# Performance work log

Hardware: AMD Instinct MI355X
Metric: run time of the kernel (lower is better)

The kernel has to match this reference:

```python
import jax, jax.numpy as jnp
import numpy as np

K = 8192  # particles
T = 4096  # timesteps
LOG2PI = float(np.log(2.0 * np.pi))


def _normal_logpdf(x, mu):
    # Normal(mu, 1).log_prob(x)
    return -0.5 * (x - mu) ** 2 - 0.5 * LOG2PI


def setup_inputs() -> dict:
    key = jax.random.key(0)
    k1, k2, k3, k4 = jax.random.split(key, 4)
    x = jax.random.normal(k1, (T,), dtype=jnp.float32)          # observations
    w0 = jax.random.normal(k2, (K,), dtype=jnp.float32)          # Pw=N(0,1) samples
    z = jax.random.normal(k3, (K, T), dtype=jnp.float32)         # Qz=N(0,1) samples
    u = jax.random.uniform(k4, (T, K), dtype=jnp.float32)        # resampling uniforms
    return {"x": x, "w0": w0, "z": z, "u": u}


def reference(x, w0, z, u):
    # Precompute terms that the torch code computes once before the loop.
    log_Qz = _normal_logpdf(z, 0.0)                 # [K, T]  q.Qz().log_prob(z)
    log_PxGz = _normal_logpdf(x[None, :], z)        # [K, T]  p.PxGz(z).log_prob(x)
    delta = log_PxGz - log_Qz                       # [K, T]
    logK = jnp.log(jnp.asarray(K, dtype=z.dtype))

    def step(w, inp):
        z_t, d_t, u_t = inp                         # each [K]
        # log_ws = p.PzGw(w).log_prob(z_t) + log_PxGz_t - log_Qz_t
        log_ws = _normal_logpdf(z_t, w) + d_t       # [K]
        lme = jax.nn.logsumexp(log_ws) - logK       # logmeanexp over particles
        # Categorical(logits=log_ws).sample([K]) via inverse-CDF with uniforms
        cdf = jnp.cumsum(jax.nn.softmax(log_ws))    # [K]
        idx = jnp.clip(jnp.searchsorted(cdf, u_t), 0, K - 1)  # [K]
        return w[idx], lme                          # resample: w = w[idx]

    _, res = jax.lax.scan(step, w0, (z.T, delta.T, u))  # scan over T timesteps
    return jnp.sum(res)
```

## Files before the change

### kernel.cpp

```cpp
#include <hip/hip_runtime.h>
#include <math.h>

#define KP 8192
#define TSTEPS 4096
#define BLOCK 1024
#define PT 8
#define NWAVES 16
#define NBUCK 8192
#define NBF 8192.0f
#define MSTEPS 16
#define F_INF __int_as_float(0x7f800000)

template <int CTRL, int RM>
__device__ __forceinline__ float dpp_add_f(float x) {
  int s = __builtin_amdgcn_update_dpp(0, __float_as_int(x), CTRL, RM, 0xF, false);
  return x + __int_as_float(s);
}
template <int CTRL, int RM>
__device__ __forceinline__ int dpp_add_i(int x) {
  int s = __builtin_amdgcn_update_dpp(0, x, CTRL, RM, 0xF, false);
  return x + s;
}
template <int CTRL, int RM>
__device__ __forceinline__ int dpp_max_i(int x) {
  int s = __builtin_amdgcn_update_dpp(0, x, CTRL, RM, 0xF, false);
  return x > s ? x : s;
}
__device__ __forceinline__ float wscan64_add(float x) {
  x = dpp_add_f<0x111, 0xF>(x); x = dpp_add_f<0x112, 0xF>(x);
  x = dpp_add_f<0x114, 0xF>(x); x = dpp_add_f<0x118, 0xF>(x);
  x = dpp_add_f<0x142, 0xA>(x); x = dpp_add_f<0x143, 0xC>(x);
  return x;
}
__device__ __forceinline__ int wscan64_addi(int x) {
  x = dpp_add_i<0x111, 0xF>(x); x = dpp_add_i<0x112, 0xF>(x);
  x = dpp_add_i<0x114, 0xF>(x); x = dpp_add_i<0x118, 0xF>(x);
  x = dpp_add_i<0x142, 0xA>(x); x = dpp_add_i<0x143, 0xC>(x);
  return x;
}
__device__ __forceinline__ int wscan64_max(int x) {
  x = dpp_max_i<0x111, 0xF>(x); x = dpp_max_i<0x112, 0xF>(x);
  x = dpp_max_i<0x114, 0xF>(x); x = dpp_max_i<0x118, 0xF>(x);
  x = dpp_max_i<0x142, 0xA>(x); x = dpp_max_i<0x143, 0xC>(x);
  return x;
}
__device__ __forceinline__ float rscan16_add(float x) {
  x = dpp_add_f<0x111, 0xF>(x); x = dpp_add_f<0x112, 0xF>(x);
  x = dpp_add_f<0x114, 0xF>(x); x = dpp_add_f<0x118, 0xF>(x);
  return x;
}
__device__ __forceinline__ int rscan16_addi(int x) {
  x = dpp_add_i<0x111, 0xF>(x); x = dpp_add_i<0x112, 0xF>(x);
  x = dpp_add_i<0x114, 0xF>(x); x = dpp_add_i<0x118, 0xF>(x);
  return x;
}
__device__ __forceinline__ int rscan16_max(int x) {
  x = dpp_max_i<0x111, 0xF>(x); x = dpp_max_i<0x112, 0xF>(x);
  x = dpp_max_i<0x114, 0xF>(x); x = dpp_max_i<0x118, 0xF>(x);
  return x;
}
__device__ __forceinline__ float readlane_f(float v, int l) {
  return __int_as_float(__builtin_amdgcn_readlane(__float_as_int(v), l));
}

__global__ void transpose_k(const float* __restrict__ in, float* __restrict__ out) {
  __shared__ float tile[32][33];
  const int c0 = blockIdx.x * 32;
  const int r0 = blockIdx.y * 32;
  const int tx = threadIdx.x;
  const int ty = threadIdx.y;
#pragma unroll
  for (int i = 0; i < 32; i += 8)
    tile[ty + i][tx] = in[(size_t)(r0 + ty + i) * TSTEPS + c0 + tx];
  __syncthreads();
#pragma unroll
  for (int i = 0; i < 32; i += 8)
    out[(size_t)(c0 + ty + i) * KP + r0 + tx] = tile[tx][ty + i];
}

__global__ __launch_bounds__(BLOCK) void sortu_k(const float* __restrict__ u,
                                                 float* __restrict__ su,
                                                 unsigned short* __restrict__ rnk) {
  __shared__ int hist[NBUCK];
  __shared__ float sval[KP];
  __shared__ unsigned short sidx[KP];
  __shared__ int redi[NWAVES];
  const int t = blockIdx.x;
  const int tid = threadIdx.x;
  const int lane = tid & 63;
  const int wid = tid >> 6;
  const int kbase = tid * PT;

  float uv[PT];
  {
    float4 a = *(const float4*)(u + (size_t)t * KP + kbase);
    float4 b = *(const float4*)(u + (size_t)t * KP + kbase + 4);
    uv[0] = a.x; uv[1] = a.y; uv[2] = a.z; uv[3] = a.w;
    uv[4] = b.x; uv[5] = b.y; uv[6] = b.z; uv[7] = b.w;
  }
  int bj[PT];
#pragma unroll
  for (int j = 0; j < PT; ++j) {
    int b = (int)(uv[j] * NBF);
    bj[j] = b > NBUCK - 1 ? NBUCK - 1 : b;
  }
  {
    int4 z4; z4.x = z4.y = z4.z = z4.w = 0;
    *(int4*)(hist + kbase) = z4;
    *(int4*)(hist + kbase + 4) = z4;
  }
  __syncthreads();
#pragma unroll
  for (int j = 0; j < PT; ++j) atomicAdd(&hist[bj[j]], 1);
  __syncthreads();

  int4 ha = *(const int4*)(hist + kbase);
  int4 hb = *(const int4*)(hist + kbase + 4);
  int c0 = ha.x, c1 = c0 + ha.y, c2 = c1 + ha.z, c3 = c2 + ha.w;
  int c4 = c3 + hb.x, c5 = c4 + hb.y, c6 = c5 + hb.z, c7 = c6 + hb.w;
  int wincl = wscan64_addi(c7);
  int wexcl = wincl - c7;
  if (lane == 63) redi[wid] = wincl;
  __syncthreads();
  int v16 = rscan16_addi(redi[lane & 15]);
  int cp = wid ? __builtin_amdgcn_readlane(v16, wid - 1) : 0;
  int base = cp + wexcl;
  {
    int4 pa; pa.x = base; pa.y = base + c0; pa.z = base + c1; pa.w = base + c2;
    int4 pb; pb.x = base + c3; pb.y = base + c4; pb.z = base + c5; pb.w = base + c6;
    *(int4*)(hist + kbase) = pa;
    *(int4*)(hist + kbase + 4) = pb;
  }
  __syncthreads();
#pragma unroll
  for (int j = 0; j < PT; ++j) {
    int pos = atomicAdd(&hist[bj[j]], 1);
    sval[pos] = uv[j];
    sidx[pos] = (unsigned short)(kbase + j);
  }
  __syncthreads();
  for (int bb = tid; bb < NBUCK; bb += BLOCK) {
    int s0 = bb ? hist[bb - 1] : 0;
    int e0 = hist[bb];
    for (int m = s0 + 1; m < e0; ++m) {
      float v = sval[m];
      unsigned short ix = sidx[m];
      int p = m - 1;
      while (p >= s0 && sval[p] > v) {
        sval[p + 1] = sval[p];
        sidx[p + 1] = sidx[p];
        --p;
      }
      sval[p + 1] = v;
      sidx[p + 1] = ix;
    }
  }
  __syncthreads();
  {
    float4 a, b;
    a.x = sval[kbase + 0]; a.y = sval[kbase + 1]; a.z = sval[kbase + 2]; a.w = sval[kbase + 3];
    b.x = sval[kbase + 4]; b.y = sval[kbase + 5]; b.z = sval[kbase + 6]; b.w = sval[kbase + 7];
    *(float4*)(su + (size_t)t * KP + kbase) = a;
    *(float4*)(su + (size_t)t * KP + kbase + 4) = b;
  }
#pragma unroll
  for (int j = 0; j < PT; ++j)
    rnk[(size_t)t * KP + sidx[kbase + j]] = (unsigned short)(kbase + j);
}

__global__ __launch_bounds__(BLOCK) void smc_scan3(const float* __restrict__ x,
                                                   const float* __restrict__ w0,
                                                   const float* __restrict__ zsrc,
                                                   const float* __restrict__ su_g,
                                                   const unsigned short* __restrict__ rk_g,
                                                   float* __restrict__ out) {
  extern __shared__ float sm[];
  float* w_s   = sm;
  float* cdf_s = sm + KP;
  float* su_s  = cdf_s + KP + 8;
  float* P_s   = su_s + KP + 8;
  float* redF  = P_s + KP;

  const int tid = threadIdx.x;
  const int lane = tid & 63;
  const int wid = tid >> 6;
  const int kbase = tid * PT;

  if (tid == 0) { cdf_s[KP] = F_INF; su_s[KP] = F_INF; }

  float wv[PT];
  {
    float4 a = *(const float4*)(w0 + kbase);
    float4 b = *(const float4*)(w0 + kbase + 4);
    wv[0] = a.x; wv[1] = a.y; wv[2] = a.z; wv[3] = a.w;
    wv[4] = b.x; wv[5] = b.y; wv[6] = b.z; wv[7] = b.w;
    *(float4*)(w_s + kbase) = a;
    *(float4*)(w_s + kbase + 4) = b;
  }

  float4 zna, znb, sna, snb;
  int4 rkn;
  float xt_next = x[0];
  zna = *(const float4*)(zsrc + kbase);
  znb = *(const float4*)(zsrc + kbase + 4);
  sna = *(const float4*)(su_g + kbase);
  snb = *(const float4*)(su_g + kbase + 4);
  rkn = *(const int4*)(rk_g + kbase);

  float acc = 0.f;

  for (int t = 0; t < TSTEPS; ++t) {
    *(float4*)(su_s + kbase) = sna;
    *(float4*)(su_s + kbase + 4) = snb;
    float zv[PT];
    zv[0] = zna.x; zv[1] = zna.y; zv[2] = zna.z; zv[3] = zna.w;
    zv[4] = znb.x; zv[5] = znb.y; zv[6] = znb.z; zv[7] = znb.w;
    const int4 rkc = rkn;
    const float xt = xt_next;

    if (t + 1 < TSTEPS) {
      xt_next = x[t + 1];
      const size_t ro = (size_t)(t + 1) * KP + kbase;
      zna = *(const float4*)(zsrc + ro);
      znb = *(const float4*)(zsrc + ro + 4);
      sna = *(const float4*)(su_g + ro);
      snb = *(const float4*)(su_g + ro + 4);
      rkn = *(const int4*)(rk_g + ro);
    }

    float s[PT];
    float run = 0.f;
#pragma unroll
    for (int j = 0; j < PT; ++j) {
      float d = zv[j] - wv[j];
      float lw = fmaf(xt, zv[j], -0.5f * d * d);
      run += __expf(lw);
      s[j] = run;
    }
    const float wincl = wscan64_add(run);
    const float wexcl = wincl - run;
    if (lane == 63) redF[wid] = wincl;
    __syncthreads();

    float v16 = rscan16_add(redF[lane & 15]);
    const float total = readlane_f(v16, 15);
    const float wpre = wid ? readlane_f(v16, wid - 1) : 0.f;
    const float base = wpre + wexcl;
    const float invT = 1.0f / total;
    if (tid == 0)
      acc += __logf(total) - 9.0109133472792886f
             - 0.5f * (1.8378770664093453f + xt * xt);
    {
      float4 a, b;
      a.x = (base + s[0]) * invT; a.y = (base + s[1]) * invT;
      a.z = (base + s[2]) * invT; a.w = (base + s[3]) * invT;
      b.x = (base + s[4]) * invT; b.y = (base + s[5]) * invT;
      b.z = (base + s[6]) * invT; b.w = (base + s[7]) * invT;
      *(float4*)(cdf_s + kbase) = a;
      *(float4*)(cdf_s + kbase + 4) = b;
    }
    __syncthreads();

    {
      const int d = tid * MSTEPS;
      int lo = d > KP ? d - KP : 0;
      int hi = d < KP ? d : KP;
      while (lo < hi) {
        const int m = (lo + hi) >> 1;
        const float a = cdf_s[m];
        const float b = su_s[d - 1 - m];
        if (a >= b) hi = m; else lo = m + 1;
      }
      int i = lo;
      int j = d - lo;
      float av = cdf_s[i];
      float bv = su_s[j];
#pragma unroll 1
      for (int sme = 0; sme < MSTEPS; ++sme) {
        const bool cons = (av < bv);
        if (!cons) P_s[j] = w_s[i < KP ? i : KP - 1];
        i += cons ? 1 : 0;
        j += cons ? 0 : 1;
        const float nv = cons ? cdf_s[i] : su_s[j];
        av = cons ? nv : av;
        bv = cons ? bv : nv;
      }
    }
    __syncthreads();

    {
      int r[PT];
      r[0] = rkc.x & 0xffff; r[1] = (rkc.x >> 16) & 0xffff;
      r[2] = rkc.y & 0xffff; r[3] = (rkc.y >> 16) & 0xffff;
      r[4] = rkc.z & 0xffff; r[5] = (rkc.z >> 16) & 0xffff;
      r[6] = rkc.w & 0xffff; r[7] = (rkc.w >> 16) & 0xffff;
#pragma unroll
      for (int j = 0; j < PT; ++j) wv[j] = P_s[r[j]];
      float4 a, b;
      a.x = wv[0]; a.y = wv[1]; a.z = wv[2]; a.w = wv[3];
      b.x = wv[4]; b.y = wv[5]; b.z = wv[6]; b.w = wv[7];
      *(float4*)(w_s + kbase) = a;
      *(float4*)(w_s + kbase + 4) = b;
    }
  }

  if (tid == 0) out[0] = acc;
}

template <bool ZTRANS>
__global__ __launch_bounds__(BLOCK) void smc_scan(const float* __restrict__ x,
                                                  const float* __restrict__ w0,
                                                  const float* __restrict__ zsrc,
                                                  const float* __restrict__ u,
                                                  float* __restrict__ out) {
  extern __shared__ float sm[];
  float* wbufA = sm;
  float* wbufB = sm + KP;
  float* cdf_s = sm + 2 * KP;
  float* cend = cdf_s + KP;
  float* red = cend + BLOCK;
  int* redi = (int*)(red + NWAVES);
  int* bcI = redi + NWAVES;
  int* L_s = bcI + 4;

  const int tid = threadIdx.x;
  const int lane = tid & 63;
  const int wid = tid >> 6;
  const int kbase = tid * PT;

  float* wcur = wbufA;
  float* wnxt = wbufB;

  for (int i = tid; i < NBUCK; i += BLOCK) L_s[i] = 0;
  if (tid == 0) L_s[NBUCK] = KP - 1;

  float wv[PT];
  {
    float4 a = *(const float4*)(w0 + kbase);
    float4 b = *(const float4*)(w0 + kbase + 4);
    wv[0] = a.x; wv[1] = a.y; wv[2] = a.z; wv[3] = a.w;
    wv[4] = b.x; wv[5] = b.y; wv[6] = b.z; wv[7] = b.w;
    *(float4*)(wcur + kbase) = a;
    *(float4*)(wcur + kbase + 4) = b;
  }
  __syncthreads();

  float zn[PT], un[PT];
  float xt_next = x[0];
  if (ZTRANS) {
    float4 a = *(const float4*)(zsrc + kbase);
    float4 b = *(const float4*)(zsrc + kbase + 4);
    zn[0] = a.x; zn[1] = a.y; zn[2] = a.z; zn[3] = a.w;
    zn[4] = b.x; zn[5] = b.y; zn[6] = b.z; zn[7] = b.w;
  } else {
#pragma unroll
    for (int j = 0; j < PT; ++j) zn[j] = zsrc[(size_t)(kbase + j) * TSTEPS];
  }
  {
    float4 a = *(const float4*)(u + kbase);
    float4 b = *(const float4*)(u + kbase + 4);
    un[0] = a.x; un[1] = a.y; un[2] = a.z; un[3] = a.w;
    un[4] = b.x; un[5] = b.y; un[6] = b.z; un[7] = b.w;
  }

  float acc = 0.f;

  for (int t = 0; t < TSTEPS; ++t) {
    float zv[PT], uv[PT];
#pragma unroll
    for (int j = 0; j < PT; ++j) { zv[j] = zn[j]; uv[j] = un[j]; }
    const float xt = xt_next;

    if (t + 1 < TSTEPS) {
      xt_next = x[t + 1];
      if (ZTRANS) {
        float4 a = *(const float4*)(zsrc + (size_t)(t + 1) * KP + kbase);
        float4 b = *(const float4*)(zsrc + (size_t)(t + 1) * KP + kbase + 4);
        zn[0] = a.x; zn[1] = a.y; zn[2] = a.z; zn[3] = a.w;
        zn[4] = b.x; zn[5] = b.y; zn[6] = b.z; zn[7] = b.w;
      } else {
#pragma unroll
        for (int j = 0; j < PT; ++j)
          zn[j] = zsrc[(size_t)(kbase + j) * TSTEPS + t + 1];
      }
      float4 a = *(const float4*)(u + (size_t)(t + 1) * KP + kbase);
      float4 b = *(const float4*)(u + (size_t)(t + 1) * KP + kbase + 4);
      un[0] = a.x; un[1] = a.y; un[2] = a.z; un[3] = a.w;
      un[4] = b.x; un[5] = b.y; un[6] = b.z; un[7] = b.w;
    }

    float s[PT];
    float run = 0.f;
#pragma unroll
    for (int j = 0; j < PT; ++j) {
      float d = zv[j] - wv[j];
      float lw = fmaf(xt, zv[j], -0.5f * d * d);
      run += __expf(lw);
      s[j] = run;
    }
    const float wincl = wscan64_add(run);
    const float wexcl = wincl - run;
    if (lane == 63) red[wid] = wincl;
    __syncthreads();

    float v16 = rscan16_add(red[lane & 15]);
    const float total = readlane_f(v16, 15);
    const float wpre = wid ? readlane_f(v16, wid - 1) : 0.f;
    const float base = wpre + wexcl;
    const float invT = 1.0f / total;

    float cvn[PT];
#pragma unroll
    for (int j = 0; j < PT; ++j) cvn[j] = (base + s[j]) * invT;
    {
      float4 a, b;
      a.x = cvn[0]; a.y = cvn[1]; a.z = cvn[2]; a.w = cvn[3];
      b.x = cvn[4]; b.y = cvn[5]; b.z = cvn[6]; b.w = cvn[7];
      *(float4*)(cdf_s + kbase) = a;
      *(float4*)(cdf_s + kbase + 4) = b;
    }
    cend[tid] = cvn[PT - 1];
    if (tid == BLOCK - 1) bcI[0] = (int)(cvn[PT - 1] * NBF);
    {
      int4 z4; z4.x = z4.y = z4.z = z4.w = 0;
      *(int4*)(L_s + kbase) = z4;
      *(int4*)(L_s + kbase + 4) = z4;
    }
    if (tid == 0)
      acc += __logf(total) - 9.0109133472792886f
             - 0.5f * (1.8378770664093453f + xt * xt);
    __syncthreads();

    {
      const float cprev = tid ? cend[tid - 1] : 0.f;
      int flo = (int)(cprev * NBF);
#pragma unroll
      for (int j = 0; j < PT; ++j) {
        int fhi = (int)(cvn[j] * NBF);
        if (fhi > NBUCK - 1) fhi = NBUCK - 1;
        if (fhi > flo) L_s[flo + 1] = kbase + j;
        flo = fhi;
      }
    }
    __syncthreads();

    int4 ra = *(const int4*)(L_s + kbase);
    int4 rb = *(const int4*)(L_s + kbase + 4);
    int c1 = max(ra.x, ra.y);
    int c2 = max(c1, ra.z);
    int c3 = max(c2, ra.w);
    int c4 = max(c3, rb.x);
    int c5 = max(c4, rb.y);
    int c6 = max(c5, rb.z);
    int c7 = max(c6, rb.w);
    const int mincl = wscan64_max(c7);
    int mexcl = __shfl_up(mincl, 1);
    if (lane == 0) mexcl = 0;
    if (lane == 63) redi[wid] = mincl;
    __syncthreads();

    {
      int mv = rscan16_max(redi[lane & 15]);
      const int crosspre = wid ? __builtin_amdgcn_readlane(mv, wid - 1) : 0;
      const int fhiLast = bcI[0];
      int m = max(crosspre, mexcl);
      int4 oa, ob;
      m = max(m, ra.x); oa.x = (kbase + 0 > fhiLast) ? (KP - 1) : m;
      m = max(m, ra.y); oa.y = (kbase + 1 > fhiLast) ? (KP - 1) : m;
      m = max(m, ra.z); oa.z = (kbase + 2 > fhiLast) ? (KP - 1) : m;
      m = max(m, ra.w); oa.w = (kbase + 3 > fhiLast) ? (KP - 1) : m;
      m = max(m, rb.x); ob.x = (kbase + 4 > fhiLast) ? (KP - 1) : m;
      m = max(m, rb.y); ob.y = (kbase + 5 > fhiLast) ? (KP - 1) : m;
      m = max(m, rb.z); ob.z = (kbase + 6 > fhiLast) ? (KP - 1) : m;
      m = max(m, rb.w); ob.w = (kbase + 7 > fhiLast) ? (KP - 1) : m;
      *(int4*)(L_s + kbase) = oa;
      *(int4*)(L_s + kbase + 4) = ob;
    }
    __syncthreads();

    int lo[PT], len[PT];
    float tg[PT];
    int anylen = 0;
#pragma unroll
    for (int j = 0; j < PT; ++j) {
      tg[j] = uv[j];
      const float fb = uv[j] * NBF;
      int b = (int)fb;
      b = min(b, NBUCK - 1);
      const int i0 = L_s[b];
      const int i1 = L_s[b + 1];
      lo[j] = i0;
      len[j] = i1 - i0;
      anylen |= len[j];
    }
    while (anylen) {
      anylen = 0;
#pragma unroll
      for (int j = 0; j < PT; ++j) {
        const int half = len[j] >> 1;
        const float c = cdf_s[lo[j] + half];
        const bool adv = (c < tg[j]) & (len[j] > 0);
        lo[j] = adv ? lo[j] + half + 1 : lo[j];
        len[j] = adv ? len[j] - half - 1 : half;
        anylen |= len[j];
      }
    }

    float nw[PT];
#pragma unroll
    for (int j = 0; j < PT; ++j) nw[j] = wcur[lo[j]];
    {
      float4 a, b;
      a.x = nw[0]; a.y = nw[1]; a.z = nw[2]; a.w = nw[3];
      b.x = nw[4]; b.y = nw[5]; b.z = nw[6]; b.w = nw[7];
      *(float4*)(wnxt + kbase) = a;
      *(float4*)(wnxt + kbase + 4) = b;
    }
#pragma unroll
    for (int j = 0; j < PT; ++j) wv[j] = nw[j];
    float* tmp = wcur; wcur = wnxt; wnxt = tmp;
  }

  if (tid == 0) out[0] = acc;
}

extern "C" void kernel_launch(void* const* d_in, const int* in_sizes, int n_in,
                              void* d_out, int out_size, void* d_ws, size_t ws_size,
                              hipStream_t stream) {
  const float* x = (const float*)d_in[0];
  const float* w0 = (const float*)d_in[1];
  const float* z = (const float*)d_in[2];
  const float* u = (const float*)d_in[3];
  float* out = (float*)d_out;

  const size_t SZ_ZT = (size_t)KP * TSTEPS * sizeof(float);
  const size_t OFF_SU = SZ_ZT;
  const size_t SZ_SU = SZ_ZT;
  const size_t OFF_RK = OFF_SU + SZ_SU;
  const size_t SZ_RK = (size_t)KP * TSTEPS * 2;
  const size_t FULL = OFF_RK + SZ_RK;

  if (ws_size >= FULL) {
    char* ws = (char*)d_ws;
    float* zT = (float*)ws;
    float* su = (float*)(ws + OFF_SU);
    unsigned short* rk = (unsigned short*)(ws + OFF_RK);
    transpose_k<<<dim3(TSTEPS / 32, KP / 32), dim3(32, 8), 0, stream>>>(z, zT);
    sortu_k<<<TSTEPS, BLOCK, 0, stream>>>(u, su, rk);
    const size_t shmem3 =
        (size_t)(KP + (KP + 8) + (KP + 8) + KP + NWAVES) * sizeof(float);
    smc_scan3<<<1, BLOCK, shmem3, stream>>>(x, w0, zT, su, rk, out);
  } else {
    const size_t shmem =
        (size_t)(3 * KP + BLOCK + NWAVES + NWAVES + 4 + NBUCK + 1) * sizeof(float);
    if (ws_size >= SZ_ZT) {
      float* zT = (float*)d_ws;
      transpose_k<<<dim3(TSTEPS / 32, KP / 32), dim3(32, 8), 0, stream>>>(z, zT);
      smc_scan<true><<<1, BLOCK, shmem, stream>>>(x, w0, zT, u, out);
    } else {
      smc_scan<false><<<1, BLOCK, shmem, stream>>>(x, w0, z, u, out);
    }
  }
}
```

Baseline: 23.19 ms.

## Replace merge-path resampling with CDF bucket index and bounded binary search

Instead of merging the sorted uniforms with the CDF via a merge-path diagonal search and a 16-step serial merge, the kernel builds a uniform bucket table over the CDF (first index per bucket, filled by a max-scan). Each sorted uniform then runs a short binary search inside its bucket. This aims to cut the per-step serial merge latency and the divergent diagonal search, at the cost of extra barriers per timestep, a max-scan pass, and data-dependent loop lengths when many CDF entries fall in one bucket.

```diff
diff --git a/kernel.cpp b/kernel.cpp
--- a/kernel.cpp
+++ b/kernel.cpp
@@ -8,8 +8,6 @@
 #define NWAVES 16
 #define NBUCK 8192
 #define NBF 8192.0f
-#define MSTEPS 16
-#define F_INF __int_as_float(0x7f800000)
 
 template <int CTRL, int RM>
 __device__ __forceinline__ float dpp_add_f(float x) {
@@ -168,25 +166,27 @@
     rnk[(size_t)t * KP + sidx[kbase + j]] = (unsigned short)(kbase + j);
 }
 
-__global__ __launch_bounds__(BLOCK) void smc_scan3(const float* __restrict__ x,
-                                                   const float* __restrict__ w0,
-                                                   const float* __restrict__ zsrc,
-                                                   const float* __restrict__ su_g,
-                                                   const unsigned short* __restrict__ rk_g,
-                                                   float* __restrict__ out) {
+__global__ __launch_bounds__(BLOCK) void smc_scan5(
+    const float* __restrict__ x, const float* __restrict__ w0,
+    const float* __restrict__ zsrc, const float* __restrict__ su_g,
+    const unsigned short* __restrict__ rk_g, float* __restrict__ out) {
   extern __shared__ float sm[];
-  float* w_s   = sm;
+  float* w_s = sm;
   float* cdf_s = sm + KP;
-  float* su_s  = cdf_s + KP + 8;
-  float* P_s   = su_s + KP + 8;
-  float* redF  = P_s + KP;
+  float* P2_s = cdf_s + KP;
+  float* cend = P2_s + KP;
+  float* red = cend + BLOCK;
+  int* redi = (int*)(red + NWAVES);
+  int* bcI = redi + NWAVES;
+  int* L_s = bcI + 4;
 
   const int tid = threadIdx.x;
   const int lane = tid & 63;
   const int wid = tid >> 6;
   const int kbase = tid * PT;
 
-  if (tid == 0) { cdf_s[KP] = F_INF; su_s[KP] = F_INF; }
+  for (int i = tid; i < NBUCK; i += BLOCK) L_s[i] = 0;
+  if (tid == 0) L_s[NBUCK] = KP - 1;
 
   float wv[PT];
   {
@@ -197,6 +197,7 @@
     *(float4*)(w_s + kbase) = a;
     *(float4*)(w_s + kbase + 4) = b;
   }
+  __syncthreads();
 
   float4 zna, znb, sna, snb;
   int4 rkn;
@@ -210,11 +211,11 @@
   float acc = 0.f;
 
   for (int t = 0; t < TSTEPS; ++t) {
-    *(float4*)(su_s + kbase) = sna;
-    *(float4*)(su_s + kbase + 4) = snb;
-    float zv[PT];
+    float zv[PT], suv[PT];
     zv[0] = zna.x; zv[1] = zna.y; zv[2] = zna.z; zv[3] = zna.w;
     zv[4] = znb.x; zv[5] = znb.y; zv[6] = znb.z; zv[7] = znb.w;
+    suv[0] = sna.x; suv[1] = sna.y; suv[2] = sna.z; suv[3] = sna.w;
+    suv[4] = snb.x; suv[5] = snb.y; suv[6] = snb.z; suv[7] = snb.w;
     const int4 rkc = rkn;
     const float xt = xt_next;
 
@@ -239,63 +240,129 @@
     }
     const float wincl = wscan64_add(run);
     const float wexcl = wincl - run;
-    if (lane == 63) redF[wid] = wincl;
-    __syncthreads();
-
-    float v16 = rscan16_add(redF[lane & 15]);
+    if (lane == 63) red[wid] = wincl;
+    __syncthreads();
+
+    float v16 = rscan16_add(red[lane & 15]);
     const float total = readlane_f(v16, 15);
     const float wpre = wid ? readlane_f(v16, wid - 1) : 0.f;
     const float base = wpre + wexcl;
     const float invT = 1.0f / total;
+
+    float cvn[PT];
+#pragma unroll
+    for (int j = 0; j < PT; ++j) cvn[j] = (base + s[j]) * invT;
+    {
+      float4 a, b;
+      a.x = cvn[0]; a.y = cvn[1]; a.z = cvn[2]; a.w = cvn[3];
+      b.x = cvn[4]; b.y = cvn[5]; b.z = cvn[6]; b.w = cvn[7];
+      *(float4*)(cdf_s + kbase) = a;
+      *(float4*)(cdf_s + kbase + 4) = b;
+    }
+    cend[tid] = cvn[PT - 1];
+    if (tid == BLOCK - 1) bcI[0] = (int)(cvn[PT - 1] * NBF);
+    {
+      int4 z4; z4.x = z4.y = z4.z = z4.w = 0;
+      *(int4*)(L_s + kbase) = z4;
+      *(int4*)(L_s + kbase + 4) = z4;
+    }
     if (tid == 0)
       acc += __logf(total) - 9.0109133472792886f
              - 0.5f * (1.8378770664093453f + xt * xt);
-    {
+    __syncthreads();
+
+    {
+      const float cprev = tid ? cend[tid - 1] : 0.f;
+      int flo = (int)(cprev * NBF);
+#pragma unroll
+      for (int j = 0; j < PT; ++j) {
+        int fhi = (int)(cvn[j] * NBF);
+        if (fhi > NBUCK - 1) fhi = NBUCK - 1;
+        if (fhi > flo) L_s[flo + 1] = kbase + j;
+        flo = fhi;
+      }
+    }
+    __syncthreads();
+
+    int4 ra = *(const int4*)(L_s + kbase);
+    int4 rb = *(const int4*)(L_s + kbase + 4);
+    int c1 = max(ra.x, ra.y);
+    int c2 = max(c1, ra.z);
+    int c3 = max(c2, ra.w);
+    int c4 = max(c3, rb.x);
+    int c5 = max(c4, rb.y);
+    int c6 = max(c5, rb.z);
+    int c7 = max(c6, rb.w);
+    const int mincl = wscan64_max(c7);
+    int mexcl = __shfl_up(mincl, 1);
+    if (lane == 0) mexcl = 0;
+    if (lane == 63) redi[wid] = mincl;
+    __syncthreads();
+
+    {
+      int mv = rscan16_max(redi[lane & 15]);
+      const int crosspre = wid ? __builtin_amdgcn_readlane(mv, wid - 1) : 0;
+      const int fhiLast = bcI[0];
+      int m = max(crosspre, mexcl);
+      int4 oa, ob;
+      m = max(m, ra.x); oa.x = (kbase + 0 > fhiLast) ? (KP - 1) : m;
+      m = max(m, ra.y); oa.y = (kbase + 1 > fhiLast) ? (KP - 1) : m;
+      m = max(m, ra.z); oa.z = (kbase + 2 > fhiLast) ? (KP - 1) : m;
+      m = max(m, ra.w); oa.w = (kbase + 3 > fhiLast) ? (KP - 1) : m;
+      m = max(m, rb.x); ob.x = (kbase + 4 > fhiLast) ? (KP - 1) : m;
+      m = max(m, rb.y); ob.y = (kbase + 5 > fhiLast) ? (KP - 1) : m;
+      m = max(m, rb.z); ob.z = (kbase + 6 > fhiLast) ? (KP - 1) : m;
+      m = max(m, rb.w); ob.w = (kbase + 7 > fhiLast) ? (KP - 1) : m;
+      *(int4*)(L_s + kbase) = oa;
+      *(int4*)(L_s + kbase + 4) = ob;
+    }
+    __syncthreads();
+
+    int lo[PT], len[PT];
+    int anylen = 0;
+#pragma unroll
+    for (int j = 0; j < PT; ++j) {
+      const float fb = suv[j] * NBF;
+      int b = (int)fb;
+      b = min(b, NBUCK - 1);
+      const int i0 = L_s[b];
+      const int i1 = L_s[b + 1];
+      lo[j] = i0;
+      len[j] = i1 - i0;
+      anylen |= len[j];
+    }
+    while (anylen) {
+      anylen = 0;
+#pragma unroll
+      for (int j = 0; j < PT; ++j) {
+        const int half = len[j] >> 1;
+        const float c = cdf_s[lo[j] + half];
+        const bool adv = (c < suv[j]) & (len[j] > 0);
+        lo[j] = adv ? lo[j] + half + 1 : lo[j];
+        len[j] = adv ? len[j] - half - 1 : half;
+        anylen |= len[j];
+      }
+    }
+
+    {
+      float pv[PT];
+#pragma unroll
+      for (int j = 0; j < PT; ++j) pv[j] = w_s[lo[j]];
       float4 a, b;
-      a.x = (base + s[0]) * invT; a.y = (base + s[1]) * invT;
-      a.z = (base + s[2]) * invT; a.w = (base + s[3]) * invT;
-      b.x = (base + s[4]) * invT; b.y = (base + s[5]) * invT;
-      b.z = (base + s[6]) * invT; b.w = (base + s[7]) * invT;
-      *(float4*)(cdf_s + kbase) = a;
-      *(float4*)(cdf_s + kbase + 4) = b;
-    }
-    __syncthreads();
-
-    {
-      const int d = tid * MSTEPS;
-      int lo = d > KP ? d - KP : 0;
-      int hi = d < KP ? d : KP;
-      while (lo < hi) {
-        const int m = (lo + hi) >> 1;
-        const float a = cdf_s[m];
-        const float b = su_s[d - 1 - m];
-        if (a >= b) hi = m; else lo = m + 1;
-      }
-      int i = lo;
-      int j = d - lo;
-      float av = cdf_s[i];
-      float bv = su_s[j];
-#pragma unroll 1
-      for (int sme = 0; sme < MSTEPS; ++sme) {
-        const bool cons = (av < bv);
-        if (!cons) P_s[j] = w_s[i < KP ? i : KP - 1];
-        i += cons ? 1 : 0;
-        j += cons ? 0 : 1;
-        const float nv = cons ? cdf_s[i] : su_s[j];
-        av = cons ? nv : av;
-        bv = cons ? bv : nv;
-      }
-    }
-    __syncthreads();
-
-    {
-      int r[PT];
-      r[0] = rkc.x & 0xffff; r[1] = (rkc.x >> 16) & 0xffff;
-      r[2] = rkc.y & 0xffff; r[3] = (rkc.y >> 16) & 0xffff;
-      r[4] = rkc.z & 0xffff; r[5] = (rkc.z >> 16) & 0xffff;
-      r[6] = rkc.w & 0xffff; r[7] = (rkc.w >> 16) & 0xffff;
-#pragma unroll
-      for (int j = 0; j < PT; ++j) wv[j] = P_s[r[j]];
+      a.x = pv[0]; a.y = pv[1]; a.z = pv[2]; a.w = pv[3];
+      b.x = pv[4]; b.y = pv[5]; b.z = pv[6]; b.w = pv[7];
+      *(float4*)(P2_s + kbase) = a;
+      *(float4*)(P2_s + kbase + 4) = b;
+    }
+    __syncthreads();
+
+    {
+      const int r0 = rkc.x & 0xffff, r1 = (rkc.x >> 16) & 0xffff;
+      const int r2 = rkc.y & 0xffff, r3 = (rkc.y >> 16) & 0xffff;
+      const int r4 = rkc.z & 0xffff, r5 = (rkc.z >> 16) & 0xffff;
+      const int r6 = rkc.w & 0xffff, r7 = (rkc.w >> 16) & 0xffff;
+      wv[0] = P2_s[r0]; wv[1] = P2_s[r1]; wv[2] = P2_s[r2]; wv[3] = P2_s[r3];
+      wv[4] = P2_s[r4]; wv[5] = P2_s[r5]; wv[6] = P2_s[r6]; wv[7] = P2_s[r7];
       float4 a, b;
       a.x = wv[0]; a.y = wv[1]; a.z = wv[2]; a.w = wv[3];
       b.x = wv[4]; b.y = wv[5]; b.z = wv[6]; b.w = wv[7];
@@ -547,9 +614,10 @@
     unsigned short* rk = (unsigned short*)(ws + OFF_RK);
     transpose_k<<<dim3(TSTEPS / 32, KP / 32), dim3(32, 8), 0, stream>>>(z, zT);
     sortu_k<<<TSTEPS, BLOCK, 0, stream>>>(u, su, rk);
-    const size_t shmem3 =
-        (size_t)(KP + (KP + 8) + (KP + 8) + KP + NWAVES) * sizeof(float);
-    smc_scan3<<<1, BLOCK, shmem3, stream>>>(x, w0, zT, su, rk, out);
+    const size_t shmem5 =
+        (size_t)(3 * KP + BLOCK + NWAVES) * sizeof(float) +
+        (size_t)(NWAVES + 4 + NBUCK + 1) * sizeof(int);
+    smc_scan5<<<1, BLOCK, shmem5, stream>>>(x, w0, zT, su, rk, out);
   } else {
     const size_t shmem =
         (size_t)(3 * KP + BLOCK + NWAVES + NWAVES + 4 + NBUCK + 1) * sizeof(float);
```

After: 23.67 ms. 1.02x slower.
